# Kernel tuning notes

Measured on AMD Instinct MI355X. Metric: run time of the kernel, lower is better.

The kernel has to match this reference:

```python
import jax, jax.numpy as jnp
import numpy as np

TOP_K = 2


def setup_inputs() -> dict:
    key = jax.random.key(0)
    k0, k1, k2, k3 = jax.random.split(key, 4)
    N, D, O, E = 131072, 512, 512, 16
    H = D // 4  # gate hidden: gate_input_size // 4
    x = jax.random.normal(k0, (N, D), dtype=jnp.float32)
    # gate MLP params (task_bh=0 gate; Linear weights stored as [in, out])
    Wg1 = jax.random.normal(k1, (D, H), dtype=jnp.float32) / np.sqrt(D).astype(np.float32)
    bg1 = jnp.zeros((H,), jnp.float32)
    Wg2 = jax.random.normal(k2, (H, E), dtype=jnp.float32) * 0.02
    bg2 = jnp.zeros((E,), jnp.float32)
    # per-expert Linear(D, O) weights stacked [E, D, O]
    We = jax.random.normal(k3, (E, D, O), dtype=jnp.float32) / np.sqrt(D).astype(np.float32)
    be = jnp.zeros((E, O), jnp.float32)
    return {"x": x, "Wg1": Wg1, "bg1": bg1, "Wg2": Wg2, "bg2": bg2,
            "We": We, "be": be, "task_bh": 0}


def reference(x, Wg1, bg1, Wg2, bg2, We, be, task_bh):
    # --- top_k_gating (noisy_gating=False path) ---
    h = jax.nn.gelu(x @ Wg1 + bg1, approximate=False)  # nn.GELU default is exact erf
    logits = h @ Wg2 + bg2                              # [N, E]
    probs = jax.nn.softmax(logits, axis=1) + 1e-4       # [N, E]
    top_g, top_i = jax.lax.top_k(probs, TOP_K)          # [N, K]
    N, E = probs.shape
    # dense gate matrix: zeros.scatter(1, top_k_indices, top_k_gates)
    gates = jnp.zeros_like(probs).at[jnp.arange(N)[:, None], top_i].set(top_g)
    # --- dispatch / per-expert GEMM / combine ---
    # Equivalent to: gather tokens per expert, expert Linear, scale by gate,
    # scatter-add back. Since gates[n, e] == 0 for unselected experts, the
    # combined output equals sum_e gates[:, e] * (x @ We[e] + be[e]).
    def body(acc, ewb):
        W_e, b_e, g_e = ewb                      # [D,O], [O], [N]
        return acc + g_e[:, None] * (x @ W_e + b_e), None
    init = jnp.zeros((N, We.shape[2]), x.dtype)
    out, _ = jax.lax.scan(body, init, (We, be, gates.T))
    return out
```

## Files before the change

kernel.cpp:

```cpp
#include <hip/hip_runtime.h>
#include <cstdint>
#include <math.h>


#define NTOK 131072
#define DDIM 512
#define NT 16

typedef short  bf16x8 __attribute__((ext_vector_type(8)));
typedef float  f32x4  __attribute__((ext_vector_type(4)));

__device__ __forceinline__ ushort f2bf(float f){
  uint u = __float_as_uint(f);
  u += 0x7fffu + ((u >> 16) & 1u);
  return (ushort)(u >> 16);
}
__device__ __forceinline__ float bf2f(ushort h){ return __uint_as_float(((uint)h) << 16); }

__device__ __forceinline__ void load_lds16(const void* g, void* l){
  __builtin_amdgcn_global_load_lds(
      (const __attribute__((address_space(1))) void*)(uintptr_t)g,
      (__attribute__((address_space(3))) void*)(uintptr_t)l, 16, 0, 0);
}

__device__ __forceinline__ f32x4 MFMA(bf16x8 a, bf16x8 b, f32x4 c){
  return __builtin_amdgcn_mfma_f32_16x16x32_bf16(a, b, c, 0, 0, 0);
}

__device__ __forceinline__ bf16x8 readF64(const char* buf, int r, int q){
  return *(const bf16x8*)(buf + r*128 + ((q ^ (r & 7)) << 4));
}
__device__ __forceinline__ bf16x8 readF32c(const char* buf, int r, int q){
  return *(const bf16x8*)(buf + r*64 + ((q ^ (r & 3)) << 4));
}

__device__ __forceinline__ void stageB32(const ushort* grow, char* lds, int tid){
  const char* gb = (const char*)grow;
  #pragma unroll
  for (int i = 0; i < 2; ++i){
    int lin = i*4096 + tid*16;
    int r = lin >> 6;
    int g = (lin >> 4) & 3;
    load_lds16(gb + r*1024 + ((g ^ (r & 3)) << 4), lds + i*4096 + ((tid >> 6) << 10));
  }
}

__device__ __forceinline__ void pack8(const float* fv, uint* ph, uint* pl){
  #pragma unroll
  for (int q=0;q<4;++q){
    float f0 = fv[2*q], f1 = fv[2*q+1];
    ushort h0 = f2bf(f0), h1 = f2bf(f1);
    ushort s0 = f2bf(f0 - bf2f(h0)), s1 = f2bf(f1 - bf2f(h1));
    ph[q] = (uint)h0 | ((uint)h1 << 16);
    pl[q] = (uint)s0 | ((uint)s1 << 16);
  }
}
__device__ __forceinline__ void writeA2p(char* hbuf, char* lbuf, int ar, int acq,
                                         const uint* ph, const uint* pl){
  int off = ar*64 + ((acq ^ (ar & 3)) << 4);
  *(uint4*)(hbuf + off) = make_uint4(ph[0],ph[1],ph[2],ph[3]);
  *(uint4*)(lbuf + off) = make_uint4(pl[0],pl[1],pl[2],pl[3]);
}

__global__ void kconv(const float* __restrict__ We, const float* __restrict__ Wg1,
                      ushort* __restrict__ Wt, ushort* __restrict__ W1h, ushort* __restrict__ W1l){
  __shared__ float sh[64*65];
  int bx = blockIdx.x, tid = threadIdx.x;
  if (bx < 1024){
    int e = bx >> 6, dt = (bx >> 3) & 7, ot = bx & 7;
    const float* src = We + (size_t)e*262144 + (size_t)dt*64*512 + ot*64;
    #pragma unroll
    for (int it=0; it<16; ++it){ int idx = it*256+tid; int dl = idx>>6, ol = idx&63;
      sh[dl*65+ol] = src[dl*512+ol]; }
    __syncthreads();
    ushort* dst = Wt + (size_t)e*262144 + (size_t)ot*64*512 + dt*64;
    #pragma unroll
    for (int it=0; it<16; ++it){ int idx = it*256+tid; int ol = idx>>6, dl = idx&63;
      dst[(size_t)ol*512+dl] = f2bf(sh[dl*65+ol]); }
  } else {
    int q = bx - 1024;
    int dt = q >> 1, ht = q & 1;
    const float* src = Wg1 + (size_t)dt*64*128 + ht*64;
    #pragma unroll
    for (int it=0; it<16; ++it){ int idx = it*256+tid; int dl = idx>>6, ol = idx&63;
      sh[dl*65+ol] = src[dl*128+ol]; }
    __syncthreads();
    #pragma unroll
    for (int it=0; it<16; ++it){ int idx = it*256+tid; int ol = idx>>6, dl = idx&63;
      float wv = sh[dl*65+ol];
      ushort hi = f2bf(wv);
      ushort lo = f2bf(wv - bf2f(hi));
      size_t o = (size_t)(ht*64+ol)*512 + dt*64+dl;
      W1h[o] = hi; W1l[o] = lo; }
  }
}

__global__ __launch_bounds__(256) void kgate(
    const float* __restrict__ x, const ushort* __restrict__ W1h, const ushort* __restrict__ W1l,
    const float* __restrict__ bg1, const float* __restrict__ Wg2, const float* __restrict__ bg2,
    ushort* __restrict__ xbf,
    int2* __restrict__ gate_e, float2* __restrict__ gate_g,
    int* __restrict__ refine_cnt, int* __restrict__ refine_list, int* __restrict__ counts)
{
  __shared__ __align__(16) char sm[49152];
  const int BOFF = 16384;
  int tid = threadIdx.x, bid = blockIdx.x;
  int lane = tid & 63, w = tid >> 6, wm = w >> 1, wn = w & 1;
  int t0 = bid * 64;
  int ar = tid >> 2, acq = tid & 3;
  const float* xrow = x + (size_t)(t0 + ar) * DDIM;
  char* xbfb = (char*)xbf;
  f32x4 acc[2][4];
  #pragma unroll
  for (int n=0;n<4;++n){
    float bb = bg1[wn*64 + n*16 + (lane & 15)];
    f32x4 z = {bb, bb, bb, bb};
    acc[0][n] = z; acc[1][n] = z;
  }
  stageB32(W1h, sm + BOFF, tid);
  stageB32(W1l, sm + BOFF + 8192, tid);
  {
    float fv[8];
    *(float4*)&fv[0] = *(const float4*)(xrow + acq*8);
    *(float4*)&fv[4] = *(const float4*)(xrow + acq*8 + 4);
    uint ph[4], pl[4];
    pack8(fv, ph, pl);
    if (xbf) *(uint4*)(xbfb + (size_t)(t0+ar)*1024 + acq*16) = make_uint4(ph[0],ph[1],ph[2],ph[3]);
    writeA2p(sm, sm + 4096, ar, acq, ph, pl);
  }
  for (int ks = 0; ks < 16; ++ks){
    int b = ks & 1;
    asm volatile("s_waitcnt vmcnt(0)" ::: "memory");
    __syncthreads();
    uint ph[4], pl[4];
    if (ks < 15){
      int k2 = ks + 1, b2 = k2 & 1;
      stageB32(W1h + k2*32, sm + BOFF + b2*16384, tid);
      stageB32(W1l + k2*32, sm + BOFF + b2*16384 + 8192, tid);
      float fv[8];
      *(float4*)&fv[0] = *(const float4*)(xrow + k2*32 + acq*8);
      *(float4*)&fv[4] = *(const float4*)(xrow + k2*32 + acq*8 + 4);
      pack8(fv, ph, pl);
      if (xbf) *(uint4*)(xbfb + (size_t)(t0+ar)*1024 + k2*64 + acq*16) = make_uint4(ph[0],ph[1],ph[2],ph[3]);
    }
    const char* Ah = sm + b*8192;
    const char* Al = Ah + 4096;
    const char* Bh = sm + BOFF + b*16384;
    const char* Bl = Bh + 8192;
    bf16x8 ah[2], alv[2], bh[4], blv[4];
    #pragma unroll
    for (int m=0;m<2;++m){
      int r = wm*32 + m*16 + (lane & 15);
      ah[m]  = readF32c(Ah, r, lane >> 4);
      alv[m] = readF32c(Al, r, lane >> 4);
    }
    #pragma unroll
    for (int n=0;n<4;++n){
      int r = wn*64 + n*16 + (lane & 15);
      bh[n]  = readF32c(Bh, r, lane >> 4);
      blv[n] = readF32c(Bl, r, lane >> 4);
    }
    #pragma unroll
    for (int m=0;m<2;++m)
      #pragma unroll
      for (int n=0;n<4;++n){
        acc[m][n] = MFMA(ah[m],  bh[n],  acc[m][n]);
        acc[m][n] = MFMA(ah[m],  blv[n], acc[m][n]);
        acc[m][n] = MFMA(alv[m], bh[n],  acc[m][n]);
      }
    if (ks < 15){
      int b2 = (ks + 1) & 1;
      writeA2p(sm + b2*8192, sm + b2*8192 + 4096, ar, acq, ph, pl);
    }
  }
  __syncthreads();
  float* hl = (float*)sm;
  #pragma unroll
  for (int m=0;m<2;++m)
    #pragma unroll
    for (int n=0;n<4;++n)
      #pragma unroll
      for (int j=0;j<4;++j){
        int row = wm*32 + m*16 + ((lane >> 4) << 2) + j;
        int col = wn*64 + n*16 + (lane & 15);
        float uv = acc[m][n][j];
        hl[row*132 + col] = 0.5f * uv * (1.0f + erff(uv * 0.70710678118654752f));
      }
  __syncthreads();
  {
    int tt = tid >> 2, cc = tid & 3;
    float4 bb = *(const float4*)(bg2 + cc*4);
    float l0 = bb.x, l1 = bb.y, l2 = bb.z, l3 = bb.w;
    const float* hrow = hl + tt*132;
    #pragma unroll 8
    for (int i = 0; i < 128; ++i){
      float hv = hrow[i];
      float4 wv = *(const float4*)(Wg2 + i*16 + cc*4);
      l0 += hv*wv.x; l1 += hv*wv.y; l2 += hv*wv.z; l3 += hv*wv.w;
    }
    float* ll = (float*)(sm + 33792);
    *(float4*)(ll + tt*16 + cc*4) = make_float4(l0, l1, l2, l3);
  }
  int* hist = (int*)(sm + 40960);
  hist[tid] = 0;
  __syncthreads();
  if (tid < 64){
    int t = t0 + tid;
    const float* l = (const float*)(sm + 33792) + tid*16;
    float b1 = -1e30f, b2 = -1e30f, b3 = -1e30f; int e1 = 0, e2 = 0;
    #pragma unroll
    for (int e = 0; e < 16; ++e){
      float v = l[e];
      if (v > b1){ b3 = b2; b2 = b1; e2 = e1; b1 = v; e1 = e; }
      else if (v > b2){ b3 = b2; b2 = v; e2 = e; }
      else if (v > b3){ b3 = v; }
    }
    double s = 0.0;
    #pragma unroll
    for (int e = 0; e < 16; ++e) s += exp((double)l[e] - (double)b1);
    double inv = 1.0 / s;
    gate_e[t] = make_int2(e1, e2);
    gate_g[t] = make_float2((float)(inv + 1e-4), (float)(exp((double)b2 - (double)b1) * inv + 1e-4));
    if (b2 - b3 < 2e-4f){
      int pos = atomicAdd(refine_cnt, 1);
      refine_list[pos] = t;
    }
    int pa = min(e1, e2), pb = max(e1, e2);
    atomicAdd(&hist[pa*16 + pb], 1);
  }
  __syncthreads();
  if (hist[tid]) atomicAdd(&counts[tid], hist[tid]);
}

__global__ __launch_bounds__(128) void krefine(
    const float* __restrict__ x, const float* __restrict__ Wg1, const float* __restrict__ bg1,
    const float* __restrict__ Wg2, const float* __restrict__ bg2,
    const int* __restrict__ refine_cnt, const int* __restrict__ refine_list,
    int2* __restrict__ gate_e, float2* __restrict__ gate_g, int* __restrict__ counts)
{
  __shared__ float  xs[512];
  __shared__ double hd[128];
  __shared__ double ld[16];
  int tid = threadIdx.x;
  int rc = *refine_cnt;
  for (int i = blockIdx.x; i < rc; i += gridDim.x){
    __syncthreads();
    int t = refine_list[i];
    *(float4*)(xs + tid*4) = *(const float4*)(x + (size_t)t*DDIM + tid*4);
    __syncthreads();
    double a = (double)bg1[tid];
    for (int d = 0; d < 512; ++d) a += (double)xs[d] * (double)Wg1[d*128 + tid];
    hd[tid] = 0.5 * a * (1.0 + erf(a * 0.70710678118654752440));
    __syncthreads();
    if (tid < 16){
      double s = (double)bg2[tid];
      for (int k = 0; k < 128; ++k) s += hd[k] * (double)Wg2[k*16 + tid];
      ld[tid] = s;
    }
    __syncthreads();
    if (tid == 0){
      int2 olde = gate_e[t];
      double b1 = -1e300, b2 = -1e300; int e1 = 0, e2 = 0;
      for (int e = 0; e < 16; ++e){
        double v = ld[e];
        if (v > b1){ b2 = b1; e2 = e1; b1 = v; e1 = e; }
        else if (v > b2){ b2 = v; e2 = e; }
      }
      double s = 0.0;
      for (int e = 0; e < 16; ++e) s += exp(ld[e] - b1);
      double inv = 1.0 / s;
      int oldp = min(olde.x, olde.y)*16 + max(olde.x, olde.y);
      int newp = min(e1, e2)*16 + max(e1, e2);
      if (oldp != newp){ atomicSub(&counts[oldp], 1); atomicAdd(&counts[newp], 1); }
      gate_e[t] = make_int2(e1, e2);
      gate_g[t] = make_float2((float)(inv + 1e-4), (float)(exp(b2 - b1) * inv + 1e-4));
    }
  }
}

__global__ void kscan(const int* __restrict__ counts, int* __restrict__ bases,
                      int* __restrict__ tile_pair, int* __restrict__ tile_row0, int* __restrict__ ntiles,
                      int ts){
  int l = threadIdx.x;
  int4 c = *(const int4*)(counts + l*4);
  int s = c.x + c.y + c.z + c.w;
  int ps = s;
  #pragma unroll
  for (int d = 1; d < 64; d <<= 1){ int v = __shfl_up(ps, d); if (l >= d) ps += v; }
  int ex = ps - s;
  bases[4*l+0] = ex;
  bases[4*l+1] = ex + c.x;
  bases[4*l+2] = ex + c.x + c.y;
  bases[4*l+3] = ex + c.x + c.y + c.z;
  if (l == 63) bases[256] = ex + s;
  int t0 = (c.x + ts-1) / ts, t1 = (c.y + ts-1) / ts, t2 = (c.z + ts-1) / ts, t3 = (c.w + ts-1) / ts;
  int tsum = t0 + t1 + t2 + t3;
  int pt = tsum;
  #pragma unroll
  for (int d = 1; d < 64; d <<= 1){ int v = __shfl_up(pt, d); if (l >= d) pt += v; }
  int ext = pt - tsum;
  if (l == 63) *ntiles = ext + tsum;
  int tb = ext;
  int cc[4] = {c.x, c.y, c.z, c.w};
  #pragma unroll
  for (int j = 0; j < 4; ++j){
    int pp = 4*l + j;
    for (int r = 0; r < cc[j]; r += ts){ tile_pair[tb] = pp; tile_row0[tb] = r; ++tb; }
  }
}

__global__ void kscatter(const int2* __restrict__ gate_e, const float2* __restrict__ gate_g,
                         const int* __restrict__ bases, int* __restrict__ cursors,
                         int* __restrict__ pair_tok, float2* __restrict__ pair_g){
  __shared__ int h[256];
  __shared__ int gb[256];
  int tid = threadIdx.x;
  h[tid] = 0; __syncthreads();
  int t = blockIdx.x*256 + tid;
  int2 ee = gate_e[t]; float2 gg = gate_g[t];
  int a, b; float ga, gbv;
  if (ee.x < ee.y){ a = ee.x; b = ee.y; ga = gg.x; gbv = gg.y; }
  else            { a = ee.y; b = ee.x; ga = gg.y; gbv = gg.x; }
  int p = a*16 + b;
  int off = atomicAdd(&h[p], 1);
  __syncthreads();
  if (h[tid]) gb[tid] = bases[tid] + atomicAdd(&cursors[tid], h[tid]);
  __syncthreads();
  int slot = gb[p] + off;
  pair_tok[slot] = t;
  pair_g[slot] = make_float2(ga, gbv);
}

#define SB0 __builtin_amdgcn_sched_barrier(0)
#define PH_MID do{ __builtin_amdgcn_s_barrier(); \
                   asm volatile("s_waitcnt lgkmcnt(0)"); SB0; }while(0)
#define PH_END do{ SB0; __builtin_amdgcn_s_barrier(); }while(0)

#define RDA(hp, mb) do{ \
  _Pragma("unroll") for (int m_=0;m_<4;++m_){ \
    int r_ = ((mb)+m_)*16 + l15; \
    af[m_][0] = readF64(hp, r_, l4); \
    af[m_][1] = readF64(hp, r_, 4+l4); }}while(0)
#define RDB(hp, bv, nb) do{ \
  _Pragma("unroll") for (int n_=0;n_<2;++n_){ \
    int r_ = bln + ((nb)+n_)*16 + l15; \
    bv[n_][0] = readF64(hp, r_, l4); \
    bv[n_][1] = readF64(hp, r_, 4+l4); }}while(0)
#define MMAC(bv, mb, nb) do{ \
  __builtin_amdgcn_s_setprio(1); \
  _Pragma("unroll") for (int m_=0;m_<4;++m_){ \
    _Pragma("unroll") for (int n_=0;n_<2;++n_){ \
      acc[(mb)+m_][(nb)+n_] = MFMA(af[m_][0], bv[n_][0], acc[(mb)+m_][(nb)+n_]); \
      acc[(mb)+m_][(nb)+n_] = MFMA(af[m_][1], bv[n_][1], acc[(mb)+m_][(nb)+n_]); }} \
  __builtin_amdgcn_s_setprio(0); \
}while(0)

__global__ __launch_bounds__(512, 2) void kexpert2(
    const ushort* __restrict__ xbf, const ushort* __restrict__ Wt, const float* __restrict__ be,
    float* __restrict__ out,
    const int* __restrict__ counts, const int* __restrict__ bases,
    const int* __restrict__ tile_pair, const int* __restrict__ tile_row0, const int* __restrict__ ntiles,
    const int* __restrict__ pair_tok, const float2* __restrict__ pair_g)
{
  __shared__ __align__(16) char sm[134144];
  const int BBASE = 65536, LTOK = 131072, LG = 132096;
  int bid = blockIdx.x;
  int tile = ((bid >> 4) << 3) | (bid & 7);
  int nt = (bid >> 3) & 1;
  if (tile >= *ntiles) return;
  int p = tile_pair[tile], row0 = tile_row0[tile];
  int base = bases[p], cnt = counts[p];
  int eA = p >> 4, eB = p & 15;
  int tid = threadIdx.x, lane = tid & 63, w = tid >> 6;
  int wm = w >> 2, wn = w & 3;
  int l15 = lane & 15, l4 = lane >> 4;
  int bln = (wn & 1) * 64;
  if (tid < 256){
    int rr = row0 + tid; bool v = rr < cnt;
    ((int*)(sm + LTOK))[tid] = v ? pair_tok[base + rr] : -1;
    ((float2*)(sm + LG))[tid] = v ? pair_g[base + rr] : make_float2(0.f, 1.f);
  }
  __syncthreads();

  int rr0 = tid >> 3;
  int sw = ((tid & 7) ^ (rr0 & 7)) << 4;
  const char* xb = (const char*)xbf;
  const char* srcA[2][2];
  #pragma unroll
  for (int h = 0; h < 2; ++h)
    #pragma unroll
    for (int i = 0; i < 2; ++i){
      int tk = ((const int*)(sm + LTOK))[h*128 + i*64 + rr0];
      if (tk < 0) tk = 0;
      srcA[h][i] = xb + (size_t)tk*1024 + sw;
    }
  const char* srcB0 = (const char*)Wt + (size_t)eA*524288 + (size_t)(nt*256 + rr0)*1024 + sw;
  long long edelt = ((long long)eB - eA) * 524288;
  char* dA = sm + w*1024;
  char* dB = sm + BBASE + w*1024;

  auto stA = [&](int t, int h){
    if (t >= NT) return;
    int ks = t & 7, bf_ = t & 1;
    load_lds16(srcA[h][0] + ks*128, dA + bf_*32768 + h*16384);
    load_lds16(srcA[h][1] + ks*128, dA + bf_*32768 + h*16384 + 8192);
  };
  auto stB = [&](int t, int h){
    if (t >= NT) return;
    int ks = t & 7, bf_ = t & 1;
    long long eo = ((t >= 8) ? edelt : 0) + ks*128;
    load_lds16(srcB0 + h*131072 + eo,         dB + bf_*32768 + h*16384);
    load_lds16(srcB0 + h*131072 + 65536 + eo, dB + bf_*32768 + h*16384 + 8192);
  };

  const char* A0 = sm + wm*16384;
  const char* A1 = A0 + 32768;
  const char* B0 = sm + BBASE + (wn >> 1)*16384;
  const char* B1 = B0 + 32768;

  f32x4 acc[8][4];
  #pragma unroll
  for (int m = 0; m < 8; ++m)
    #pragma unroll
    for (int n = 0; n < 4; ++n) acc[m][n] = (f32x4){0.f,0.f,0.f,0.f};

  stA(0,0); stA(0,1); stB(0,0); stB(0,1); stB(1,0); stB(1,1);
  asm volatile("s_waitcnt vmcnt(4)"); SB0;
  __builtin_amdgcn_s_barrier();

  bf16x8 af[4][2], bL[2][2], bH[2][2];
  #pragma unroll 1
  for (int i = 0; i < 8; ++i){
    int t0 = 2*i, t1 = t0 + 1;
    RDA(A0, 0); RDB(B0, bL, 0); stA(t1, 0);
    PH_MID; MMAC(bL, 0, 0); PH_END;
    RDB(B0, bH, 2); stA(t1, 1);
    PH_MID; MMAC(bH, 0, 2); PH_END;
    RDA(A0, 4); stB(t0+2, 0);
    PH_MID; MMAC(bH, 4, 2); PH_END;
    stB(t0+2, 1);
    if (i != 7) { asm volatile("s_waitcnt vmcnt(4)"); SB0; }
    else        { asm volatile("s_waitcnt vmcnt(0)"); SB0; }
    PH_MID; MMAC(bL, 4, 0); PH_END;
    RDA(A1, 0); RDB(B1, bL, 0); stA(t0+2, 0);
    PH_MID; MMAC(bL, 0, 0); PH_END;
    RDB(B1, bH, 2); stA(t0+2, 1);
    PH_MID; MMAC(bH, 0, 2); PH_END;
    RDA(A1, 4); stB(t1+2, 0);
    PH_MID; MMAC(bH, 4, 2); PH_END;
    stB(t1+2, 1);
    if (i != 7) { asm volatile("s_waitcnt vmcnt(4)"); SB0; }
    PH_MID; MMAC(bL, 4, 0); PH_END;
    if (i == 3){
      #pragma unroll
      for (int m = 0; m < 8; ++m)
        #pragma unroll
        for (int j = 0; j < 4; ++j){
          int row = wm*128 + m*16 + l4*4 + j;
          float2 g2 = ((const float2*)(sm + LG))[row];
          float r_ = g2.x / g2.y;
          #pragma unroll
          for (int n = 0; n < 4; ++n) acc[m][n][j] *= r_;
        }
    }
  }

  float bcA[4], bcB[4];
  #pragma unroll
  for (int n = 0; n < 4; ++n){
    int col = nt*256 + wn*64 + n*16 + l15;
    bcA[n] = be[(size_t)eA*DDIM + col];
    bcB[n] = be[(size_t)eB*DDIM + col];
  }
  #pragma unroll
  for (int m = 0; m < 8; ++m)
    #pragma unroll
    for (int j = 0; j < 4; ++j){
      int row = wm*128 + m*16 + l4*4 + j;
      int tk = ((const int*)(sm + LTOK))[row];
      if (tk >= 0){
        float2 g2 = ((const float2*)(sm + LG))[row];
        float* orow = out + (size_t)tk*DDIM + nt*256 + wn*64;
        #pragma unroll
        for (int n = 0; n < 4; ++n)
          orow[n*16 + l15] = g2.y*acc[m][n][j] + g2.x*bcA[n] + g2.y*bcB[n];
      }
    }
}

__global__ __launch_bounds__(256, 2) void kexpertF(
    const float* __restrict__ x,
    const ushort* __restrict__ Wt, const float* __restrict__ be,
    float* __restrict__ out,
    const int* __restrict__ counts, const int* __restrict__ bases,
    const int* __restrict__ tile_pair, const int* __restrict__ tile_row0, const int* __restrict__ ntiles,
    const int* __restrict__ pair_tok, const float2* __restrict__ pair_g)
{
  __shared__ __align__(16) char sm[67072];
  const int ABUF = 0, BBUF = 32768, LTOK = 65536, LGOFF = 66048;
  int tile = blockIdx.x >> 2, nt = blockIdx.x & 3;
  if (tile >= *ntiles) return;
  int p = tile_pair[tile], row0 = tile_row0[tile];
  int base = bases[p], cnt = counts[p];
  int eA = p >> 4, eB = p & 15;
  int tid = threadIdx.x, lane = tid & 63;
  int w = tid >> 6, wm = w >> 1, wn = w & 1;
  if (tid < 128){
    int rr = row0 + tid; bool v = rr < cnt;
    ((int*)(sm + LTOK))[tid] = v ? pair_tok[base + rr] : -1;
    ((float2*)(sm + LGOFF))[tid] = v ? pair_g[base + rr] : make_float2(0.f, 0.f);
  }
  __syncthreads();
  const char* wb = (const char*)Wt;
  int grp = tid >> 3, gch = tid & 7;
  int swz = (gch ^ (grp & 7)) << 4;
  long long edelt = ((long long)eB - (long long)eA) * 524288;
  const char* srcB[4];
  #pragma unroll
  for (int i = 0; i < 4; ++i)
    srcB[i] = wb + (long long)eA*524288 + (size_t)(nt*128 + i*32 + grp)*1024 + swz;
  int arow = tid >> 1, ach = tid & 1;
  int tkr = ((const int*)(sm + LTOK))[arow];
  if (tkr < 0) tkr = 0;
  const float* xrow = x + (size_t)tkr*DDIM + ach*32;
  int ldst = (w << 10);
  #pragma unroll
  for (int i = 0; i < 4; ++i) load_lds16(srcB[i], sm + BBUF + i*4096 + ldst);
  {
    uint pk[16];
    #pragma unroll
    for (int q2 = 0; q2 < 4; ++q2){
      float4 fv = *(const float4*)(xrow + q2*8);
      float4 fw = *(const float4*)(xrow + q2*8 + 4);
      pk[q2*4+0] = (uint)f2bf(fv.x) | ((uint)f2bf(fv.y) << 16);
      pk[q2*4+1] = (uint)f2bf(fv.z) | ((uint)f2bf(fv.w) << 16);
      pk[q2*4+2] = (uint)f2bf(fw.x) | ((uint)f2bf(fw.y) << 16);
      pk[q2*4+3] = (uint)f2bf(fw.z) | ((uint)f2bf(fw.w) << 16);
    }
    #pragma unroll
    for (int q2 = 0; q2 < 4; ++q2){
      int g = ach*4 + q2;
      *(uint4*)(sm + ABUF + arow*128 + ((g ^ (arow & 7)) << 4)) =
          make_uint4(pk[q2*4], pk[q2*4+1], pk[q2*4+2], pk[q2*4+3]);
    }
  }
  f32x4 acc[4][4], res[4][4];
  #pragma unroll
  for (int m=0;m<4;++m)
    #pragma unroll
    for (int n=0;n<4;++n) acc[m][n] = (f32x4){0.f,0.f,0.f,0.f};
  for (int u = 0; u < 16; ++u){
    int b = u & 1;
    asm volatile("s_waitcnt vmcnt(0)" ::: "memory");
    __syncthreads();
    int un = u + 1;
    uint pk[16];
    if (un < 16){
      int b2 = un & 1;
      long long aoff = (long long)(un & 7) * 128;
      long long boff = aoff + ((un >> 3) ? edelt : 0);
      #pragma unroll
      for (int i = 0; i < 4; ++i)
        load_lds16(srcB[i] + boff, sm + BBUF + b2*16384 + i*4096 + ldst);
      const float* xr = xrow + (un & 7)*64;
      #pragma unroll
      for (int q2 = 0; q2 < 4; ++q2){
        float4 fv = *(const float4*)(xr + q2*8);
        float4 fw = *(const float4*)(xr + q2*8 + 4);
        pk[q2*4+0] = (uint)f2bf(fv.x) | ((uint)f2bf(fv.y) << 16);
        pk[q2*4+1] = (uint)f2bf(fv.z) | ((uint)f2bf(fv.w) << 16);
        pk[q2*4+2] = (uint)f2bf(fw.x) | ((uint)f2bf(fw.y) << 16);
        pk[q2*4+3] = (uint)f2bf(fw.z) | ((uint)f2bf(fw.w) << 16);
      }
    }
    const char* Ab = sm + ABUF + b*16384;
    const char* Bb = sm + BBUF + b*16384;
    bf16x8 af2[4][2], bf2[4][2];
    #pragma unroll
    for (int m=0;m<4;++m){
      int r = wm*64 + m*16 + (lane & 15);
      af2[m][0] = readF64(Ab, r, (lane >> 4));
      af2[m][1] = readF64(Ab, r, 4 + (lane >> 4));
    }
    #pragma unroll
    for (int n=0;n<4;++n){
      int r = wn*64 + n*16 + (lane & 15);
      bf2[n][0] = readF64(Bb, r, (lane >> 4));
      bf2[n][1] = readF64(Bb, r, 4 + (lane >> 4));
    }
    #pragma unroll
    for (int m=0;m<4;++m)
      #pragma unroll
      for (int n=0;n<4;++n){
        acc[m][n] = MFMA(af2[m][0], bf2[n][0], acc[m][n]);
        acc[m][n] = MFMA(af2[m][1], bf2[n][1], acc[m][n]);
      }
    if (un < 16){
      int b2 = un & 1;
      #pragma unroll
      for (int q2 = 0; q2 < 4; ++q2){
        int g = ach*4 + q2;
        *(uint4*)(sm + ABUF + b2*16384 + arow*128 + ((g ^ (arow & 7)) << 4)) =
            make_uint4(pk[q2*4], pk[q2*4+1], pk[q2*4+2], pk[q2*4+3]);
      }
    }
    if (u == 7){
      const float* bev = be + (size_t)eA*DDIM + nt*128;
      float bcol[4];
      #pragma unroll
      for (int n=0;n<4;++n) bcol[n] = bev[wn*64 + n*16 + (lane & 15)];
      #pragma unroll
      for (int m=0;m<4;++m)
        #pragma unroll
        for (int j=0;j<4;++j){
          int row = wm*64 + m*16 + ((lane >> 4) << 2) + j;
          float g = ((const float2*)(sm + LGOFF))[row].x;
          #pragma unroll
          for (int n=0;n<4;++n){
            res[m][n][j] = g * (acc[m][n][j] + bcol[n]);
            acc[m][n][j] = 0.f;
          }
        }
    }
    if (u == 15){
      const float* bev = be + (size_t)eB*DDIM + nt*128;
      float bcol[4];
      #pragma unroll
      for (int n=0;n<4;++n) bcol[n] = bev[wn*64 + n*16 + (lane & 15)];
      #pragma unroll
      for (int m=0;m<4;++m)
        #pragma unroll
        for (int j=0;j<4;++j){
          int row = wm*64 + m*16 + ((lane >> 4) << 2) + j;
          int tk = ((const int*)(sm + LTOK))[row];
          float g = ((const float2*)(sm + LGOFF))[row].y;
          if (tk >= 0){
            float* orow = out + (size_t)tk*DDIM + nt*128;
            #pragma unroll
            for (int n=0;n<4;++n)
              orow[wn*64 + n*16 + (lane & 15)] = res[m][n][j] + g * (acc[m][n][j] + bcol[n]);
          }
        }
    }
  }
}

extern "C" void kernel_launch(void* const* d_in, const int* in_sizes, int n_in,
                              void* d_out, int out_size, void* d_ws, size_t ws_size,
                              hipStream_t stream)
{
  const float* x   = (const float*)d_in[0];
  const float* Wg1 = (const float*)d_in[1];
  const float* bg1 = (const float*)d_in[2];
  const float* Wg2 = (const float*)d_in[3];
  const float* bg2 = (const float*)d_in[4];
  const float* We  = (const float*)d_in[5];
  const float* be  = (const float*)d_in[6];
  float* out = (float*)d_out;
  char* ws = (char*)d_ws;

  ushort* Wt        = (ushort*)(ws + 0);
  ushort* W1h       = (ushort*)(ws + 8388608);
  ushort* W1l       = (ushort*)(ws + 8519680);
  char*   CTRL      = ws + 8650752;
  int*  refine_cnt  = (int*)(CTRL);
  int*  ntiles      = (int*)(CTRL + 4);
  int*  counts      = (int*)(CTRL + 64);
  int*  cursors     = (int*)(CTRL + 2048);
  int*  bases       = (int*)(CTRL + 4096);
  int2*   gate_e    = (int2*)(ws + 8658944);
  float2* gate_g    = (float2*)(ws + 9707520);
  int*  refine_list = (int*)(ws + 10756096);
  int*  pair_tok    = (int*)(ws + 11280384);
  float2* pair_g    = (float2*)(ws + 11804672);
  int*  tile_pair   = (int*)(ws + 12853248);
  int*  tile_row0   = (int*)(ws + 12863488);
  const size_t XBF_OFF = 16777216ull;
  const size_t XBF_BYTES = (size_t)NTOK * DDIM * 2;
  bool bf16a = ws_size >= XBF_OFF + XBF_BYTES;
  ushort* xbf = bf16a ? (ushort*)(ws + XBF_OFF) : nullptr;

  hipMemsetAsync(CTRL, 0, 8192, stream);
  hipLaunchKernelGGL(kconv,    dim3(1040), dim3(256), 0, stream, We, Wg1, Wt, W1h, W1l);
  hipLaunchKernelGGL(kgate,    dim3(2048), dim3(256), 0, stream, x, W1h, W1l, bg1, Wg2, bg2,
                     xbf, gate_e, gate_g, refine_cnt, refine_list, counts);
  hipLaunchKernelGGL(krefine,  dim3(512),  dim3(128), 0, stream, x, Wg1, bg1, Wg2, bg2,
                     refine_cnt, refine_list, gate_e, gate_g, counts);
  hipLaunchKernelGGL(kscan,    dim3(1),    dim3(64),  0, stream, counts, bases, tile_pair, tile_row0, ntiles,
                     bf16a ? 256 : 128);
  hipLaunchKernelGGL(kscatter, dim3(512),  dim3(256), 0, stream, gate_e, gate_g, bases, cursors, pair_tok, pair_g);
  if (bf16a)
    hipLaunchKernelGGL(kexpert2, dim3(1408), dim3(512), 0, stream, xbf, Wt, be, out,
                       counts, bases, tile_pair, tile_row0, ntiles, pair_tok, pair_g);
  else
    hipLaunchKernelGGL(kexpertF, dim3(5120), dim3(256), 0, stream, x, Wt, be, out,
                       counts, bases, tile_pair, tile_row0, ntiles, pair_tok, pair_g);
  (void)in_sizes; (void)n_in; (void)out_size; (void)ws_size;
}
```

Measured before the change: 445.4 us.

## Switch gate and expert GEMMs from split-bf16 to fp16 MFMA

Replaces the bf16 hi/lo split (three MFMAs per step) in the gate GEMM with a single fp16 MFMA, and moves the expert GEMMs and activation copy to fp16. The second gate layer (h @ Wg2) becomes an MFMA using an fp16 fragment layout of Wg2 built in the conversion kernel. To cover the lower gate precision, the near-tie threshold for exact fp32 refinement is widened and the refine kernel gets more blocks. This trades gate-path MFMA work and LDS traffic for more tokens going through the refine pass, plus fp16 range risk.

Measured after the change: 482.5 us. +8.3%, slower.

```diff
diff --git a/kernel.cpp b/kernel.cpp
--- a/kernel.cpp
+++ b/kernel.cpp
@@ -7,15 +7,9 @@
 #define DDIM 512
 #define NT 16
 
-typedef short  bf16x8 __attribute__((ext_vector_type(8)));
-typedef float  f32x4  __attribute__((ext_vector_type(4)));
-
-__device__ __forceinline__ ushort f2bf(float f){
-  uint u = __float_as_uint(f);
-  u += 0x7fffu + ((u >> 16) & 1u);
-  return (ushort)(u >> 16);
-}
-__device__ __forceinline__ float bf2f(ushort h){ return __uint_as_float(((uint)h) << 16); }
+typedef _Float16 f16;
+typedef f16   f16x8 __attribute__((ext_vector_type(8)));
+typedef float f32x4 __attribute__((ext_vector_type(4)));
 
 __device__ __forceinline__ void load_lds16(const void* g, void* l){
   __builtin_amdgcn_global_load_lds(
@@ -23,18 +17,24 @@
       (__attribute__((address_space(3))) void*)(uintptr_t)l, 16, 0, 0);
 }
 
-__device__ __forceinline__ f32x4 MFMA(bf16x8 a, bf16x8 b, f32x4 c){
-  return __builtin_amdgcn_mfma_f32_16x16x32_bf16(a, b, c, 0, 0, 0);
-}
-
-__device__ __forceinline__ bf16x8 readF64(const char* buf, int r, int q){
-  return *(const bf16x8*)(buf + r*128 + ((q ^ (r & 7)) << 4));
-}
-__device__ __forceinline__ bf16x8 readF32c(const char* buf, int r, int q){
-  return *(const bf16x8*)(buf + r*64 + ((q ^ (r & 3)) << 4));
-}
-
-__device__ __forceinline__ void stageB32(const ushort* grow, char* lds, int tid){
+__device__ __forceinline__ f32x4 MFMAH(f16x8 a, f16x8 b, f32x4 c){
+  return __builtin_amdgcn_mfma_f32_16x16x32_f16(a, b, c, 0, 0, 0);
+}
+
+__device__ __forceinline__ f16x8 readF64h(const char* buf, int r, int q){
+  return *(const f16x8*)(buf + r*128 + ((q ^ (r & 7)) << 4));
+}
+__device__ __forceinline__ f16x8 readF32h(const char* buf, int r, int q){
+  return *(const f16x8*)(buf + r*64 + ((q ^ (r & 3)) << 4));
+}
+__device__ __forceinline__ f16x8 pack8f(const float* fv){
+  f16x8 v;
+  #pragma unroll
+  for (int j=0;j<8;++j) v[j] = (f16)fv[j];
+  return v;
+}
+
+__device__ __forceinline__ void stageB32(const void* grow, char* lds, int tid){
   const char* gb = (const char*)grow;
   #pragma unroll
   for (int i = 0; i < 2; ++i){
@@ -45,25 +45,9 @@
   }
 }
 
-__device__ __forceinline__ void pack8(const float* fv, uint* ph, uint* pl){
-  #pragma unroll
-  for (int q=0;q<4;++q){
-    float f0 = fv[2*q], f1 = fv[2*q+1];
-    ushort h0 = f2bf(f0), h1 = f2bf(f1);
-    ushort s0 = f2bf(f0 - bf2f(h0)), s1 = f2bf(f1 - bf2f(h1));
-    ph[q] = (uint)h0 | ((uint)h1 << 16);
-    pl[q] = (uint)s0 | ((uint)s1 << 16);
-  }
-}
-__device__ __forceinline__ void writeA2p(char* hbuf, char* lbuf, int ar, int acq,
-                                         const uint* ph, const uint* pl){
-  int off = ar*64 + ((acq ^ (ar & 3)) << 4);
-  *(uint4*)(hbuf + off) = make_uint4(ph[0],ph[1],ph[2],ph[3]);
-  *(uint4*)(lbuf + off) = make_uint4(pl[0],pl[1],pl[2],pl[3]);
-}
-
 __global__ void kconv(const float* __restrict__ We, const float* __restrict__ Wg1,
-                      ushort* __restrict__ Wt, ushort* __restrict__ W1h, ushort* __restrict__ W1l){
+                      const float* __restrict__ Wg2,
+                      f16* __restrict__ Wt, f16* __restrict__ W1, char* __restrict__ Wg2f){
   __shared__ float sh[64*65];
   int bx = blockIdx.x, tid = threadIdx.x;
   if (bx < 1024){
@@ -73,11 +57,11 @@
     for (int it=0; it<16; ++it){ int idx = it*256+tid; int dl = idx>>6, ol = idx&63;
       sh[dl*65+ol] = src[dl*512+ol]; }
     __syncthreads();
-    ushort* dst = Wt + (size_t)e*262144 + (size_t)ot*64*512 + dt*64;
+    f16* dst = Wt + (size_t)e*262144 + (size_t)ot*64*512 + dt*64;
     #pragma unroll
     for (int it=0; it<16; ++it){ int idx = it*256+tid; int ol = idx>>6, dl = idx&63;
-      dst[(size_t)ol*512+dl] = f2bf(sh[dl*65+ol]); }
-  } else {
+      dst[(size_t)ol*512+dl] = (f16)sh[dl*65+ol]; }
+  } else if (bx < 1040){
     int q = bx - 1024;
     int dt = q >> 1, ht = q & 1;
     const float* src = Wg1 + (size_t)dt*64*128 + ht*64;
@@ -87,25 +71,29 @@
     __syncthreads();
     #pragma unroll
     for (int it=0; it<16; ++it){ int idx = it*256+tid; int ol = idx>>6, dl = idx&63;
-      float wv = sh[dl*65+ol];
-      ushort hi = f2bf(wv);
-      ushort lo = f2bf(wv - bf2f(hi));
-      size_t o = (size_t)(ht*64+ol)*512 + dt*64+dl;
-      W1h[o] = hi; W1l[o] = lo; }
+      W1[(size_t)(ht*64+ol)*512 + dt*64+dl] = (f16)sh[dl*65+ol]; }
+  } else {
+    int ks = tid >> 6, l = tid & 63;
+    int col = l & 15, kb = ks*32 + ((l >> 4) << 3);
+    f16x8 v;
+    #pragma unroll
+    for (int j=0;j<8;++j) v[j] = (f16)Wg2[(kb+j)*16 + col];
+    *(f16x8*)(Wg2f + (ks*64+l)*16) = v;
   }
 }
 
 __global__ __launch_bounds__(256) void kgate(
-    const float* __restrict__ x, const ushort* __restrict__ W1h, const ushort* __restrict__ W1l,
-    const float* __restrict__ bg1, const float* __restrict__ Wg2, const float* __restrict__ bg2,
-    ushort* __restrict__ xbf,
+    const float* __restrict__ x, const f16* __restrict__ W1, const char* __restrict__ Wg2f,
+    const float* __restrict__ bg1, const float* __restrict__ bg2,
+    f16* __restrict__ xbf,
     int2* __restrict__ gate_e, float2* __restrict__ gate_g,
     int* __restrict__ refine_cnt, int* __restrict__ refine_list, int* __restrict__ counts)
 {
-  __shared__ __align__(16) char sm[49152];
-  const int BOFF = 16384;
+  __shared__ __align__(16) char sm[38912];
+  const int BOFF = 8192;
   int tid = threadIdx.x, bid = blockIdx.x;
   int lane = tid & 63, w = tid >> 6, wm = w >> 1, wn = w & 1;
+  int l15 = lane & 15, l4 = lane >> 4;
   int t0 = bid * 64;
   int ar = tid >> 2, acq = tid & 3;
   const float* xrow = x + (size_t)(t0 + ar) * DDIM;
@@ -113,67 +101,53 @@
   f32x4 acc[2][4];
   #pragma unroll
   for (int n=0;n<4;++n){
-    float bb = bg1[wn*64 + n*16 + (lane & 15)];
+    float bb = bg1[wn*64 + n*16 + l15];
     f32x4 z = {bb, bb, bb, bb};
     acc[0][n] = z; acc[1][n] = z;
   }
-  stageB32(W1h, sm + BOFF, tid);
-  stageB32(W1l, sm + BOFF + 8192, tid);
+  stageB32(W1, sm + BOFF, tid);
   {
     float fv[8];
     *(float4*)&fv[0] = *(const float4*)(xrow + acq*8);
     *(float4*)&fv[4] = *(const float4*)(xrow + acq*8 + 4);
-    uint ph[4], pl[4];
-    pack8(fv, ph, pl);
-    if (xbf) *(uint4*)(xbfb + (size_t)(t0+ar)*1024 + acq*16) = make_uint4(ph[0],ph[1],ph[2],ph[3]);
-    writeA2p(sm, sm + 4096, ar, acq, ph, pl);
+    f16x8 v8 = pack8f(fv);
+    if (xbf) *(f16x8*)(xbfb + (size_t)(t0+ar)*1024 + acq*16) = v8;
+    *(f16x8*)(sm + ar*64 + ((acq ^ (ar & 3)) << 4)) = v8;
   }
   for (int ks = 0; ks < 16; ++ks){
     int b = ks & 1;
     asm volatile("s_waitcnt vmcnt(0)" ::: "memory");
     __syncthreads();
-    uint ph[4], pl[4];
+    f16x8 v8;
     if (ks < 15){
       int k2 = ks + 1, b2 = k2 & 1;
-      stageB32(W1h + k2*32, sm + BOFF + b2*16384, tid);
-      stageB32(W1l + k2*32, sm + BOFF + b2*16384 + 8192, tid);
+      stageB32((const char*)W1 + k2*64, sm + BOFF + b2*8192, tid);
       float fv[8];
       *(float4*)&fv[0] = *(const float4*)(xrow + k2*32 + acq*8);
       *(float4*)&fv[4] = *(const float4*)(xrow + k2*32 + acq*8 + 4);
-      pack8(fv, ph, pl);
-      if (xbf) *(uint4*)(xbfb + (size_t)(t0+ar)*1024 + k2*64 + acq*16) = make_uint4(ph[0],ph[1],ph[2],ph[3]);
-    }
-    const char* Ah = sm + b*8192;
-    const char* Al = Ah + 4096;
-    const char* Bh = sm + BOFF + b*16384;
-    const char* Bl = Bh + 8192;
-    bf16x8 ah[2], alv[2], bh[4], blv[4];
-    #pragma unroll
-    for (int m=0;m<2;++m){
-      int r = wm*32 + m*16 + (lane & 15);
-      ah[m]  = readF32c(Ah, r, lane >> 4);
-      alv[m] = readF32c(Al, r, lane >> 4);
-    }
-    #pragma unroll
-    for (int n=0;n<4;++n){
-      int r = wn*64 + n*16 + (lane & 15);
-      bh[n]  = readF32c(Bh, r, lane >> 4);
-      blv[n] = readF32c(Bl, r, lane >> 4);
-    }
+      v8 = pack8f(fv);
+      if (xbf) *(f16x8*)(xbfb + (size_t)(t0+ar)*1024 + k2*64 + acq*16) = v8;
+    }
+    const char* Ab = sm + b*4096;
+    const char* Bb = sm + BOFF + b*8192;
+    f16x8 ah[2], bh[4];
+    #pragma unroll
+    for (int m=0;m<2;++m) ah[m] = readF32h(Ab, wm*32 + m*16 + l15, l4);
+    #pragma unroll
+    for (int n=0;n<4;++n) bh[n] = readF32h(Bb, wn*64 + n*16 + l15, l4);
     #pragma unroll
     for (int m=0;m<2;++m)
       #pragma unroll
-      for (int n=0;n<4;++n){
-        acc[m][n] = MFMA(ah[m],  bh[n],  acc[m][n]);
-        acc[m][n] = MFMA(ah[m],  blv[n], acc[m][n]);
-        acc[m][n] = MFMA(alv[m], bh[n],  acc[m][n]);
-      }
+      for (int n=0;n<4;++n) acc[m][n] = MFMAH(ah[m], bh[n], acc[m][n]);
     if (ks < 15){
       int b2 = (ks + 1) & 1;
-      writeA2p(sm + b2*8192, sm + b2*8192 + 4096, ar, acq, ph, pl);
-    }
-  }
-  __syncthreads();
+      *(f16x8*)(sm + b2*4096 + ar*64 + ((acq ^ (ar & 3)) << 4)) = v8;
+    }
+  }
+  __syncthreads();
+  uint4 wgf[4];
+  #pragma unroll
+  for (int ksq=0; ksq<4; ++ksq) wgf[ksq] = *(const uint4*)(Wg2f + (ksq*64+lane)*16);
   float* hl = (float*)sm;
   #pragma unroll
   for (int m=0;m<2;++m)
@@ -181,27 +155,28 @@
     for (int n=0;n<4;++n)
       #pragma unroll
       for (int j=0;j<4;++j){
-        int row = wm*32 + m*16 + ((lane >> 4) << 2) + j;
-        int col = wn*64 + n*16 + (lane & 15);
+        int row = wm*32 + m*16 + (l4 << 2) + j;
+        int col = wn*64 + n*16 + l15;
         float uv = acc[m][n][j];
         hl[row*132 + col] = 0.5f * uv * (1.0f + erff(uv * 0.70710678118654752f));
       }
   __syncthreads();
   {
-    int tt = tid >> 2, cc = tid & 3;
-    float4 bb = *(const float4*)(bg2 + cc*4);
-    float l0 = bb.x, l1 = bb.y, l2 = bb.z, l3 = bb.w;
-    const float* hrow = hl + tt*132;
-    #pragma unroll 8
-    for (int i = 0; i < 128; ++i){
-      float hv = hrow[i];
-      float4 wv = *(const float4*)(Wg2 + i*16 + cc*4);
-      l0 += hv*wv.x; l1 += hv*wv.y; l2 += hv*wv.z; l3 += hv*wv.w;
+    float bb2 = bg2[l15];
+    f32x4 acc2 = {bb2, bb2, bb2, bb2};
+    #pragma unroll
+    for (int ksq=0; ksq<4; ++ksq){
+      const float* hp = (const float*)sm + (w*16 + l15)*132 + ksq*32 + l4*8;
+      f16x8 afr;
+      #pragma unroll
+      for (int j=0;j<8;++j) afr[j] = (f16)hp[j];
+      acc2 = MFMAH(afr, *(const f16x8*)&wgf[ksq], acc2);
     }
     float* ll = (float*)(sm + 33792);
-    *(float4*)(ll + tt*16 + cc*4) = make_float4(l0, l1, l2, l3);
-  }
-  int* hist = (int*)(sm + 40960);
+    #pragma unroll
+    for (int j=0;j<4;++j) ll[(w*16 + l4*4 + j)*16 + l15] = acc2[j];
+  }
+  int* hist = (int*)(sm + 37888);
   hist[tid] = 0;
   __syncthreads();
   if (tid < 64){
@@ -221,7 +196,7 @@
     double inv = 1.0 / s;
     gate_e[t] = make_int2(e1, e2);
     gate_g[t] = make_float2((float)(inv + 1e-4), (float)(exp((double)b2 - (double)b1) * inv + 1e-4));
-    if (b2 - b3 < 2e-4f){
+    if (b2 - b3 < 2e-3f){
       int pos = atomicAdd(refine_cnt, 1);
       refine_list[pos] = t;
     }
@@ -339,24 +314,24 @@
 #define RDA(hp, mb) do{ \
   _Pragma("unroll") for (int m_=0;m_<4;++m_){ \
     int r_ = ((mb)+m_)*16 + l15; \
-    af[m_][0] = readF64(hp, r_, l4); \
-    af[m_][1] = readF64(hp, r_, 4+l4); }}while(0)
+    af[m_][0] = readF64h(hp, r_, l4); \
+    af[m_][1] = readF64h(hp, r_, 4+l4); }}while(0)
 #define RDB(hp, bv, nb) do{ \
   _Pragma("unroll") for (int n_=0;n_<2;++n_){ \
     int r_ = bln + ((nb)+n_)*16 + l15; \
-    bv[n_][0] = readF64(hp, r_, l4); \
-    bv[n_][1] = readF64(hp, r_, 4+l4); }}while(0)
+    bv[n_][0] = readF64h(hp, r_, l4); \
+    bv[n_][1] = readF64h(hp, r_, 4+l4); }}while(0)
 #define MMAC(bv, mb, nb) do{ \
   __builtin_amdgcn_s_setprio(1); \
   _Pragma("unroll") for (int m_=0;m_<4;++m_){ \
     _Pragma("unroll") for (int n_=0;n_<2;++n_){ \
-      acc[(mb)+m_][(nb)+n_] = MFMA(af[m_][0], bv[n_][0], acc[(mb)+m_][(nb)+n_]); \
-      acc[(mb)+m_][(nb)+n_] = MFMA(af[m_][1], bv[n_][1], acc[(mb)+m_][(nb)+n_]); }} \
+      acc[(mb)+m_][(nb)+n_] = MFMAH(af[m_][0], bv[n_][0], acc[(mb)+m_][(nb)+n_]); \
+      acc[(mb)+m_][(nb)+n_] = MFMAH(af[m_][1], bv[n_][1], acc[(mb)+m_][(nb)+n_]); }} \
   __builtin_amdgcn_s_setprio(0); \
 }while(0)
 
 __global__ __launch_bounds__(512, 2) void kexpert2(
-    const ushort* __restrict__ xbf, const ushort* __restrict__ Wt, const float* __restrict__ be,
+    const f16* __restrict__ xbf, const f16* __restrict__ Wt, const float* __restrict__ be,
     float* __restrict__ out,
     const int* __restrict__ counts, const int* __restrict__ bases,
     const int* __restrict__ tile_pair, const int* __restrict__ tile_row0, const int* __restrict__ ntiles,
@@ -428,7 +403,7 @@
   asm volatile("s_waitcnt vmcnt(4)"); SB0;
   __builtin_amdgcn_s_barrier();
 
-  bf16x8 af[4][2], bL[2][2], bH[2][2];
+  f16x8 af[4][2], bL[2][2], bH[2][2];
   #pragma unroll 1
   for (int i = 0; i < 8; ++i){
     int t0 = 2*i, t1 = t0 + 1;
@@ -490,7 +465,7 @@
 
 __global__ __launch_bounds__(256, 2) void kexpertF(
     const float* __restrict__ x,
-    const ushort* __restrict__ Wt, const float* __restrict__ be,
+    const f16* __restrict__ Wt, const float* __restrict__ be,
     float* __restrict__ out,
     const int* __restrict__ counts, const int* __restrict__ bases,
     const int* __restrict__ tile_pair, const int* __restrict__ tile_row0, const int* __restrict__ ntiles,
@@ -527,21 +502,14 @@
   #pragma unroll
   for (int i = 0; i < 4; ++i) load_lds16(srcB[i], sm + BBUF + i*4096 + ldst);
   {
-    uint pk[16];
     #pragma unroll
     for (int q2 = 0; q2 < 4; ++q2){
-      float4 fv = *(const float4*)(xrow + q2*8);
-      float4 fw = *(const float4*)(xrow + q2*8 + 4);
-      pk[q2*4+0] = (uint)f2bf(fv.x) | ((uint)f2bf(fv.y) << 16);
-      pk[q2*4+1] = (uint)f2bf(fv.z) | ((uint)f2bf(fv.w) << 16);
-      pk[q2*4+2] = (uint)f2bf(fw.x) | ((uint)f2bf(fw.y) << 16);
-      pk[q2*4+3] = (uint)f2bf(fw.z) | ((uint)f2bf(fw.w) << 16);
-    }
-    #pragma unroll
-    for (int q2 = 0; q2 < 4; ++q2){
+      float fv[8];
+      *(float4*)&fv[0] = *(const float4*)(xrow + q2*8);
+      *(float4*)&fv[4] = *(const float4*)(xrow + q2*8 + 4);
+      f16x8 hv = pack8f(fv);
       int g = ach*4 + q2;
-      *(uint4*)(sm + ABUF + arow*128 + ((g ^ (arow & 7)) << 4)) =
-          make_uint4(pk[q2*4], pk[q2*4+1], pk[q2*4+2], pk[q2*4+3]);
+      *(f16x8*)(sm + ABUF + arow*128 + ((g ^ (arow & 7)) << 4)) = hv;
     }
   }
   f32x4 acc[4][4], res[4][4];
@@ -554,7 +522,7 @@
     asm volatile("s_waitcnt vmcnt(0)" ::: "memory");
     __syncthreads();
     int un = u + 1;
-    uint pk[16];
+    f16x8 hv[4];
     if (un < 16){
       int b2 = un & 1;
       long long aoff = (long long)(un & 7) * 128;
@@ -565,43 +533,40 @@
       const float* xr = xrow + (un & 7)*64;
       #pragma unroll
       for (int q2 = 0; q2 < 4; ++q2){
-        float4 fv = *(const float4*)(xr + q2*8);
-        float4 fw = *(const float4*)(xr + q2*8 + 4);
-        pk[q2*4+0] = (uint)f2bf(fv.x) | ((uint)f2bf(fv.y) << 16);
-        pk[q2*4+1] = (uint)f2bf(fv.z) | ((uint)f2bf(fv.w) << 16);
-        pk[q2*4+2] = (uint)f2bf(fw.x) | ((uint)f2bf(fw.y) << 16);
-        pk[q2*4+3] = (uint)f2bf(fw.z) | ((uint)f2bf(fw.w) << 16);
+        float fv[8];
+        *(float4*)&fv[0] = *(const float4*)(xr + q2*8);
+        *(float4*)&fv[4] = *(const float4*)(xr + q2*8 + 4);
+        hv[q2] = pack8f(fv);
       }
     }
     const char* Ab = sm + ABUF + b*16384;
     const char* Bb = sm + BBUF + b*16384;
-    bf16x8 af2[4][2], bf2[4][2];
+    f16x8 af2[4][2], bf2[4][2];
     #pragma unroll
     for (int m=0;m<4;++m){
       int r = wm*64 + m*16 + (lane & 15);
-      af2[m][0] = readF64(Ab, r, (lane >> 4));
-      af2[m][1] = readF64(Ab, r, 4 + (lane >> 4));
+      af2[m][0] = readF64h(Ab, r, (lane >> 4));
+      af2[m][1] = readF64h(Ab, r, 4 + (lane >> 4));
     }
     #pragma unroll
     for (int n=0;n<4;++n){
       int r = wn*64 + n*16 + (lane & 15);
-      bf2[n][0] = readF64(Bb, r, (lane >> 4));
-      bf2[n][1] = readF64(Bb, r, 4 + (lane >> 4));
+      bf2[n][0] = readF64h(Bb, r, (lane >> 4));
+      bf2[n][1] = readF64h(Bb, r, 4 + (lane >> 4));
     }
     #pragma unroll
     for (int m=0;m<4;++m)
       #pragma unroll
       for (int n=0;n<4;++n){
-        acc[m][n] = MFMA(af2[m][0], bf2[n][0], acc[m][n]);
-        acc[m][n] = MFMA(af2[m][1], bf2[n][1], acc[m][n]);
+        acc[m][n] = MFMAH(af2[m][0], bf2[n][0], acc[m][n]);
+        acc[m][n] = MFMAH(af2[m][1], bf2[n][1], acc[m][n]);
       }
     if (un < 16){
       int b2 = un & 1;
       #pragma unroll
       for (int q2 = 0; q2 < 4; ++q2){
         int g = ach*4 + q2;
-        *(uint4*)(sm + ABUF + b2*16384 + arow*128 + ((g ^ (arow & 7)) << 4)) =
-            make_uint4(pk[q2*4], pk[q2*4+1], pk[q2*4+2], pk[q2*4+3]);
+        *(f16x8*)(sm + ABUF + b2*16384 + arow*128 + ((g ^ (arow & 7)) << 4)) = hv[q2];
       }
     }
     if (u == 7){
@@ -659,10 +624,10 @@
   float* out = (float*)d_out;
   char* ws = (char*)d_ws;
 
-  ushort* Wt        = (ushort*)(ws + 0);
-  ushort* W1h       = (ushort*)(ws + 8388608);
-  ushort* W1l       = (ushort*)(ws + 8519680);
-  char*   CTRL      = ws + 8650752;
+  f16*  Wt          = (f16*)(ws + 0);
+  f16*  W1          = (f16*)(ws + 8388608);
+  char* Wg2f        = ws + 8519680;
+  char* CTRL        = ws + 8650752;
   int*  refine_cnt  = (int*)(CTRL);
   int*  ntiles      = (int*)(CTRL + 4);
   int*  counts      = (int*)(CTRL + 64);
@@ -678,13 +643,13 @@
   const size_t XBF_OFF = 16777216ull;
   const size_t XBF_BYTES = (size_t)NTOK * DDIM * 2;
   bool bf16a = ws_size >= XBF_OFF + XBF_BYTES;
-  ushort* xbf = bf16a ? (ushort*)(ws + XBF_OFF) : nullptr;
+  f16* xbf = bf16a ? (f16*)(ws + XBF_OFF) : nullptr;
 
   hipMemsetAsync(CTRL, 0, 8192, stream);
-  hipLaunchKernelGGL(kconv,    dim3(1040), dim3(256), 0, stream, We, Wg1, Wt, W1h, W1l);
-  hipLaunchKernelGGL(kgate,    dim3(2048), dim3(256), 0, stream, x, W1h, W1l, bg1, Wg2, bg2,
+  hipLaunchKernelGGL(kconv,    dim3(1041), dim3(256), 0, stream, We, Wg1, Wg2, Wt, W1, Wg2f);
+  hipLaunchKernelGGL(kgate,    dim3(2048), dim3(256), 0, stream, x, W1, Wg2f, bg1, bg2,
                      xbf, gate_e, gate_g, refine_cnt, refine_list, counts);
-  hipLaunchKernelGGL(krefine,  dim3(512),  dim3(128), 0, stream, x, Wg1, bg1, Wg2, bg2,
+  hipLaunchKernelGGL(krefine,  dim3(1024), dim3(128), 0, stream, x, Wg1, bg1, Wg2, bg2,
                      refine_cnt, refine_list, gate_e, gate_g, counts);
   hipLaunchKernelGGL(kscan,    dim3(1),    dim3(64),  0, stream, counts, bases, tile_pair, tile_row0, ntiles,
                      bf16a ? 256 : 128);
```
